# Optimization experiments

Hardware: AMD Instinct MI355X
Metric: run time of the kernel (lower is better)

The kernel has to match this reference:

```python
import jax, jax.numpy as jnp
import numpy as np
import math

NUM_HEADS = 16
HIDDEN = 1024
HEAD = HIDDEN // NUM_HEADS


def setup_inputs() -> dict:
    key = jax.random.key(0)
    ks = jax.random.split(key, 11)
    B, S, H = 2, 2048, HIDDEN
    s = 1.0 / math.sqrt(H)
    return {
        "q": jax.random.normal(ks[0], (B, S, H), jnp.float32),
        "k": jax.random.normal(ks[1], (B, S, H), jnp.float32),
        "v": jax.random.normal(ks[2], (B, S, H), jnp.float32),
        "Wq": jax.random.normal(ks[3], (H, H), jnp.float32) * s,
        "bq": jnp.zeros((H,), jnp.float32),
        "Wk": jax.random.normal(ks[4], (H, H), jnp.float32) * s,
        "bk": jnp.zeros((H,), jnp.float32),
        "Wv": jax.random.normal(ks[5], (H, H), jnp.float32) * s,
        "bv": jnp.zeros((H,), jnp.float32),
        "Wo": jax.random.normal(ks[6], (H, H), jnp.float32) * s,
        "bo": jnp.zeros((H,), jnp.float32),
    }


def reference(q, k, v, Wq, bq, Wk, bk, Wv, bv, Wo, bo):
    B, S, H = q.shape
    nh, hd = NUM_HEADS, HEAD
    # projections (torch Linear: x @ W.T + b)
    qp = (q @ Wq.T + bq).reshape(B, S, nh, hd).transpose(0, 2, 1, 3)  # [B,nh,S,hd]
    kp = (k @ Wk.T + bk).reshape(B, S, nh, hd).transpose(0, 2, 1, 3)
    vp = (v @ Wv.T + bv).reshape(B, S, nh, hd).transpose(0, 2, 1, 3)
    scores = jnp.einsum('bhqd,bhkd->bhqk', qp, kp) / math.sqrt(hd)
    attn = jax.nn.softmax(scores, axis=-1)  # [B,nh,S,S]
    o = jnp.einsum('bhqk,bhkd->bhqd', attn, vp)
    o = o.transpose(0, 2, 1, 3).reshape(B, S, H)
    return o @ Wo.T + bo
```

## Files before the change

### kernel.cpp

```cpp
#include <hip/hip_runtime.h>
#include <cstdint>
#include <type_traits>
#include <utility>

typedef __attribute__((ext_vector_type(8))) short short8;
typedef __attribute__((ext_vector_type(8))) _Float16 f16x8_t;
typedef __attribute__((ext_vector_type(4))) float f32x4;

template <typename V, typename = void>
struct mfma_h_takes : std::false_type {};
template <typename V>
struct mfma_h_takes<V, std::void_t<decltype(__builtin_amdgcn_mfma_f32_16x16x32_f16(
    std::declval<V>(), std::declval<V>(), std::declval<f32x4>(), 0, 0, 0))>>
    : std::true_type {};

using hfrag_t = std::conditional_t<mfma_h_takes<f16x8_t>::value, f16x8_t, short8>;
static_assert(mfma_h_takes<f16x8_t>::value || mfma_h_takes<short8>::value,
              "no usable mfma_f32_16x16x32_f16 signature");

__device__ __forceinline__ f32x4 mfma16h(hfrag_t a, hfrag_t b, f32x4 c) {
  return __builtin_amdgcn_mfma_f32_16x16x32_f16(a, b, c, 0, 0, 0);
}

__device__ __forceinline__ void gld_lds16(const void* g, void* l) {
  __builtin_amdgcn_global_load_lds(
      (const __attribute__((address_space(1))) void*)(uintptr_t)g,
      (__attribute__((address_space(3))) void*)(uint32_t)(uintptr_t)l, 16, 0, 0);
}

__device__ __forceinline__ uint16_t f16_rne(float x) {
  return __builtin_bit_cast(uint16_t, (_Float16)x);
}
__device__ __forceinline__ float f16_up(uint16_t h) {
  return (float)__builtin_bit_cast(_Float16, h);
}

__device__ __forceinline__ float exp2_fast(float x) {
#if __has_builtin(__builtin_amdgcn_exp2f)
  return __builtin_amdgcn_exp2f(x);
#else
  return exp2f(x);
#endif
}
__device__ __forceinline__ uint32_t pk_f16(float a, float b) {
#if __has_builtin(__builtin_amdgcn_cvt_pkrtz)
  return __builtin_bit_cast(uint32_t, __builtin_amdgcn_cvt_pkrtz(a, b));
#else
  union { uint16_t u[2]; uint32_t w; } r;
  r.u[0] = f16_rne(fminf(a, 65504.0f));
  r.u[1] = f16_rne(fminf(b, 65504.0f));
  return r.w;
#endif
}

__device__ __forceinline__ void lds_barrier() {
  asm volatile("s_waitcnt lgkmcnt(0)" ::: "memory");
  __builtin_amdgcn_sched_barrier(0);
  __builtin_amdgcn_s_barrier();
  __builtin_amdgcn_sched_barrier(0);
}

__device__ __forceinline__ int swz(int row, int col) {
  return row * 64 + ((((col >> 3) + row) & 7) << 3) + (col & 7);
}

struct SplitArgs {
  const float* src[4];
  uint16_t* hi[4];
  uint16_t* lo[4];
  int n4;
};
__global__ void split_multi(SplitArgs a) {
  const int z = blockIdx.y;
  int i = blockIdx.x * 256 + threadIdx.x;
  if (i >= a.n4) return;
  float4 x = ((const float4*)a.src[z])[i];
  ushort4 h;
  h.x = f16_rne(x.x);
  h.y = f16_rne(x.y);
  h.z = f16_rne(x.z);
  h.w = f16_rne(x.w);
  ((ushort4*)a.hi[z])[i] = h;
  if (a.lo[z]) {
    ushort4 l;
    l.x = f16_rne(x.x - f16_up(h.x));
    l.y = f16_rne(x.y - f16_up(h.y));
    l.z = f16_rne(x.z - f16_up(h.z));
    l.w = f16_rne(x.w - f16_up(h.w));
    ((ushort4*)a.lo[z])[i] = l;
  }
}

struct QKVArgs {
  const uint16_t* Ah[3];
  const uint16_t* Bh[3];
  const float* bias[3];
  uint16_t* oH[3];
  uint16_t* oL[3];
};

__global__ __launch_bounds__(256, 3) void gemm_qkv(QKVArgs args) {
  __shared__ uint16_t lds[2][2][128][32];
  const int K = 1024;
  const int tid = threadIdx.x;
  const int wv = tid >> 6, lane = tid & 63;
  const int lm = lane & 15, g = lane >> 4;
  const int wm = (wv & 1) * 64, wn = (wv >> 1) * 64;
  const int z = blockIdx.z;
  const bool isT = (z == 2);
  const int t = blockIdx.x + 8 * blockIdx.y;
  const int kx = t & 7, j = t >> 3;
  const int sx = (j & 3) | ((kx & 1) << 2);
  const int sy = (j >> 2) | ((kx >> 1) << 3);
  const int gm0 = (isT ? sx : sy) * 128;
  const int gn0 = (isT ? sy : sx) * 128;

  const uint16_t* base[2] = {args.Ah[z] + (size_t)gm0 * K,
                             args.Bh[z] + (size_t)gn0 * K};
  const int rl = lane >> 2;
  const int scl = (((lane & 3) - (rl >> 1)) & 3) * 8;
  const int ucol = ((g + (lm >> 1)) & 3) * 8;

  f32x4 acc[4][4];
#pragma unroll
  for (int a = 0; a < 4; ++a)
#pragma unroll
    for (int b = 0; b < 4; ++b) acc[a][b] = (f32x4)0.0f;

#pragma unroll
  for (int jj = 0; jj < 4; ++jj) {
    const int c = wv + 4 * jj;
    const int p = c >> 3, r16 = (c & 7) * 16;
    gld_lds16(base[p] + (size_t)(r16 + rl) * K + 0 + scl, &lds[0][p][r16][0]);
  }

#pragma unroll 1
  for (int ti = 0; ti < 32; ++ti) {
    const int cur = ti & 1;
    if (ti + 1 < 32) {
      const int kt = (ti + 1) * 32;
#pragma unroll
      for (int jj = 0; jj < 4; ++jj) {
        const int c = wv + 4 * jj;
        const int p = c >> 3, r16 = (c & 7) * 16;
        gld_lds16(base[p] + (size_t)(r16 + rl) * K + kt + scl,
                  &lds[cur ^ 1][p][r16][0]);
      }
      asm volatile("s_waitcnt vmcnt(4)" ::: "memory");
    } else {
      asm volatile("s_waitcnt vmcnt(0)" ::: "memory");
    }
    __builtin_amdgcn_sched_barrier(0);
    __builtin_amdgcn_s_barrier();
    __builtin_amdgcn_sched_barrier(0);
    hfrag_t af[4];
#pragma unroll
    for (int mf = 0; mf < 4; ++mf) {
      af[mf] = *(const hfrag_t*)&lds[cur][0][wm + mf * 16 + lm][ucol];
    }
#pragma unroll
    for (int nf = 0; nf < 4; ++nf) {
      hfrag_t bhf = *(const hfrag_t*)&lds[cur][1][wn + nf * 16 + lm][ucol];
#pragma unroll
      for (int mf = 0; mf < 4; ++mf) {
        acc[mf][nf] = mfma16h(af[mf], bhf, acc[mf][nf]);
      }
    }
    __builtin_amdgcn_sched_barrier(0);
    __builtin_amdgcn_s_barrier();
    __builtin_amdgcn_sched_barrier(0);
  }
  const float* bias = args.bias[z];
  uint16_t* oH = args.oH[z];
  uint16_t* oL = args.oL[z];
  const float kQScale = 0.18033688f;
#pragma unroll
  for (int mf = 0; mf < 4; ++mf) {
#pragma unroll
    for (int nf = 0; nf < 4; ++nf) {
      const int col = gn0 + wn + nf * 16 + lm;
#pragma unroll
      for (int i = 0; i < 4; ++i) {
        const int row = gm0 + wm + mf * 16 + g * 4 + i;
        float v = acc[mf][nf][i] + (isT ? bias[row] : bias[col]);
        if (z == 0) v *= kQScale;
        uint16_t h = f16_rne(v);
        size_t addr;
        if (!isT) {
          addr = ((size_t)((row >> 11) * 16 + (col >> 6)) * 2048 + (row & 2047)) * 64 +
                 (col & 63);
        } else {
          addr = ((size_t)((col >> 11) * 1024 + row)) * 2048 + (col & 2047);
        }
        oH[addr] = h;
        if (oL) oL[addr] = f16_rne(v - f16_up(h));
      }
    }
  }
}

__global__ __launch_bounds__(256, 2) void gemm_o(
    const uint16_t* __restrict__ Ah, const uint16_t* __restrict__ Bh,
    const float* __restrict__ bias, float* __restrict__ out) {
  const int K = 1024, N = 1024;
  __shared__ uint16_t ldsA[2][64][64];
  __shared__ uint16_t ldsB[2][128][64];
  const int tid = threadIdx.x;
  const int wv = tid >> 6, lane = tid & 63;
  const int lm = lane & 15, g = lane >> 4;
  const int wm = (wv & 1) * 32, wn = (wv >> 1) * 64;
  const int t = blockIdx.x + 8 * blockIdx.y;
  const int kx = t & 7, j = t >> 3;
  const int sx = (j & 3) | ((kx & 1) << 2);
  const int sy = (j >> 2) | ((kx >> 1) << 4);
  const int gm0 = sy * 64, gn0 = sx * 128;
  const uint16_t* baseA = Ah + (size_t)gm0 * K;
  const uint16_t* baseB = Bh + (size_t)gn0 * K;
  const int rl8 = lane >> 3;
  const int scl = (((lane & 7) - rl8) & 7) * 8;

  f32x4 acc[2][4];
#pragma unroll
  for (int a = 0; a < 2; ++a)
#pragma unroll
    for (int b = 0; b < 4; ++b) acc[a][b] = (f32x4)0.0f;

#pragma unroll
  for (int jj = 0; jj < 6; ++jj) {
    const int c = wv + 4 * jj;
    if (c < 8) {
      gld_lds16(baseA + (size_t)(c * 8 + rl8) * K + 0 + scl, &ldsA[0][c * 8][0]);
    } else {
      const int b = c - 8;
      gld_lds16(baseB + (size_t)(b * 8 + rl8) * K + 0 + scl, &ldsB[0][b * 8][0]);
    }
  }

#pragma unroll 1
  for (int ti = 0; ti < 16; ++ti) {
    const int cur = ti & 1;
    if (ti + 1 < 16) {
      const int kt = (ti + 1) * 64;
#pragma unroll
      for (int jj = 0; jj < 6; ++jj) {
        const int c = wv + 4 * jj;
        if (c < 8) {
          gld_lds16(baseA + (size_t)(c * 8 + rl8) * K + kt + scl,
                    &ldsA[cur ^ 1][c * 8][0]);
        } else {
          const int b = c - 8;
          gld_lds16(baseB + (size_t)(b * 8 + rl8) * K + kt + scl,
                    &ldsB[cur ^ 1][b * 8][0]);
        }
      }
      asm volatile("s_waitcnt vmcnt(6)" ::: "memory");
    } else {
      asm volatile("s_waitcnt vmcnt(0)" ::: "memory");
    }
    __builtin_amdgcn_sched_barrier(0);
    __builtin_amdgcn_s_barrier();
    __builtin_amdgcn_sched_barrier(0);
#pragma unroll
    for (int ks = 0; ks < 2; ++ks) {
      const int uc = ((ks * 4 + g + lm) & 7) * 8;
      hfrag_t af[2];
#pragma unroll
      for (int mf = 0; mf < 2; ++mf) {
        af[mf] = *(const hfrag_t*)&ldsA[cur][wm + mf * 16 + lm][uc];
      }
#pragma unroll
      for (int nf = 0; nf < 4; ++nf) {
        hfrag_t bhf = *(const hfrag_t*)&ldsB[cur][wn + nf * 16 + lm][uc];
#pragma unroll
        for (int mf = 0; mf < 2; ++mf) {
          acc[mf][nf] = mfma16h(af[mf], bhf, acc[mf][nf]);
        }
      }
    }
    __builtin_amdgcn_sched_barrier(0);
    __builtin_amdgcn_s_barrier();
    __builtin_amdgcn_sched_barrier(0);
  }
#pragma unroll
  for (int mf = 0; mf < 2; ++mf)
#pragma unroll
    for (int nf = 0; nf < 4; ++nf) {
      const int col = gn0 + wn + nf * 16 + lm;
#pragma unroll
      for (int i = 0; i < 4; ++i) {
        const int row = gm0 + wm + mf * 16 + g * 4 + i;
        out[(size_t)row * N + col] = acc[mf][nf][i] + bias[col];
      }
    }
}

__global__ __launch_bounds__(256, 2) void attn_kernel(
    const uint16_t* __restrict__ Qh,
    const uint16_t* __restrict__ Kh,
    const uint16_t* __restrict__ Vh,
    float* __restrict__ opart, float* __restrict__ lpart) {
  __shared__ uint16_t kt[4096];
  __shared__ uint16_t vt[4096];
  __shared__ uint16_t pp[8192];
  const int tid = threadIdx.x;
  const int wave = tid >> 6, lane = tid & 63;
  const int lm = lane & 15, g = lane >> 4;
  const int linear = blockIdx.x + 32 * blockIdx.y;
  const int bh = (linear & 7) + 8 * (linear >> 8);
  const int qt = (linear >> 3) & 15;
  const int half = (linear >> 7) & 1;
  const int kvh = half * 1024;
  const size_t base = (size_t)bh * 131072;
  const int q0 = qt * 128 + wave * 32;

  hfrag_t qf[2][2];
#pragma unroll
  for (int b = 0; b < 2; ++b) {
    const size_t rb = base + (size_t)(q0 + b * 16 + lm) * 64 + g * 8;
    qf[b][0] = *(const hfrag_t*)(Qh + rb);
    qf[b][1] = *(const hfrag_t*)(Qh + rb + 32);
  }
  f32x4 oacc[2][4];
  f32x4 lacc[2];
#pragma unroll
  for (int mf = 0; mf < 2; ++mf) {
    lacc[mf] = (f32x4)0.0f;
#pragma unroll
    for (int nf = 0; nf < 4; ++nf) oacc[mf][nf] = (f32x4)0.0f;
  }
  short8 ones_s = (short8)(short)0x3C00;
  hfrag_t ones = __builtin_bit_cast(hfrag_t, ones_s);

  const int sr = tid >> 3;
  const int sc = (tid & 7) * 8;

  uint4 kr0, kr1, vr0, vr1;
  {
    const size_t ka = base + (size_t)(kvh + sr) * 64 + sc;
    kr0 = *(const uint4*)(Kh + ka);
    kr1 = *(const uint4*)(Kh + ka + 2048);
  }

#pragma unroll 1
  for (int it = 0; it < 16; ++it) {
    const int kv0 = kvh + it * 64;
    *(uint4*)&kt[swz(sr, sc)] = kr0;
    *(uint4*)&kt[swz(sr + 32, sc)] = kr1;
    lds_barrier();
    {
      const size_t va = base + (size_t)sr * 2048 + kv0 + sc;
      vr0 = *(const uint4*)(Vh + va);
      vr1 = *(const uint4*)(Vh + va + 65536);
    }
    if (it + 1 < 16) {
      const size_t ka = base + (size_t)(kv0 + 64 + sr) * 64 + sc;
      kr0 = *(const uint4*)(Kh + ka);
      kr1 = *(const uint4*)(Kh + ka + 2048);
    }
    f32x4 sct[4][2];
#pragma unroll
    for (int a = 0; a < 4; ++a)
#pragma unroll
      for (int b = 0; b < 2; ++b) sct[a][b] = (f32x4)0.0f;
    __builtin_amdgcn_s_setprio(1);
#pragma unroll
    for (int ks = 0; ks < 2; ++ks) {
#pragma unroll
      for (int a = 0; a < 4; ++a) {
        hfrag_t kfh = *(const hfrag_t*)&kt[swz(a * 16 + lm, ks * 32 + g * 8)];
#pragma unroll
        for (int b = 0; b < 2; ++b) {
          sct[a][b] = mfma16h(kfh, qf[b][ks], sct[a][b]);
        }
      }
    }
    __builtin_amdgcn_s_setprio(0);
#pragma unroll
    for (int a = 0; a < 4; ++a) {
#pragma unroll
      for (int b = 0; b < 2; ++b) {
        float e0 = exp2_fast(sct[a][b][0]);
        float e1 = exp2_fast(sct[a][b][1]);
        float e2 = exp2_fast(sct[a][b][2]);
        float e3 = exp2_fast(sct[a][b][3]);
        uint2 pk;
        pk.x = pk_f16(e0, e1);
        pk.y = pk_f16(e2, e3);
        *(uint2*)&pp[swz(wave * 32 + b * 16 + lm, a * 16 + g * 4)] = pk;
      }
    }
    *(uint4*)&vt[swz(sr, sc)] = vr0;
    *(uint4*)&vt[swz(sr + 32, sc)] = vr1;
    lds_barrier();
    __builtin_amdgcn_s_setprio(1);
#pragma unroll
    for (int ks = 0; ks < 2; ++ks) {
      hfrag_t pa[2];
#pragma unroll
      for (int mf = 0; mf < 2; ++mf) {
        pa[mf] = *(const hfrag_t*)&pp[swz(wave * 32 + mf * 16 + lm, ks * 32 + g * 8)];
        lacc[mf] = mfma16h(pa[mf], ones, lacc[mf]);
      }
#pragma unroll
      for (int nf = 0; nf < 4; ++nf) {
        hfrag_t vbh = *(const hfrag_t*)&vt[swz(nf * 16 + lm, ks * 32 + g * 8)];
#pragma unroll
        for (int mf = 0; mf < 2; ++mf) {
          oacc[mf][nf] = mfma16h(pa[mf], vbh, oacc[mf][nf]);
        }
      }
    }
    __builtin_amdgcn_s_setprio(0);
  }
  const int obase = (half * 32 + bh) * 2048;
#pragma unroll
  for (int mf = 0; mf < 2; ++mf) {
#pragma unroll
    for (int i = 0; i < 4; ++i) {
      const int qrow = qt * 128 + wave * 32 + mf * 16 + g * 4 + i;
      float* orow = opart + ((size_t)obase + qrow) * 64;
#pragma unroll
      for (int nf = 0; nf < 4; ++nf) orow[nf * 16 + lm] = oacc[mf][nf][i];
      if (lm == 0) lpart[obase + qrow] = lacc[mf][i];
    }
  }
}

__global__ void combine_kernel(const float* __restrict__ opart,
                               const float* __restrict__ lpart,
                               uint16_t* __restrict__ oh) {
  const int idx = blockIdx.x * 256 + threadIdx.x;
  const float4 a = ((const float4*)opart)[idx];
  const float4 b = ((const float4*)(opart + 4194304))[idx];
  const int row = idx >> 4;
  const float linv = 1.0f / (lpart[row] + lpart[65536 + row]);
  const int bh = row >> 11, qq = row & 2047;
  const int bb = bh >> 4, hh = bh & 15;
  const size_t o = ((size_t)(bb * 2048 + qq)) * 1024 + hh * 64 + (idx & 15) * 4;
  ushort4 H;
  H.x = f16_rne((a.x + b.x) * linv);
  H.y = f16_rne((a.y + b.y) * linv);
  H.z = f16_rne((a.z + b.z) * linv);
  H.w = f16_rne((a.w + b.w) * linv);
  *(ushort4*)(oh + o) = H;
}

extern "C" void kernel_launch(void* const* d_in, const int* in_sizes, int n_in,
                              void* d_out, int out_size, void* d_ws, size_t ws_size,
                              hipStream_t stream) {
  const float* q = (const float*)d_in[0];
  const float* k = (const float*)d_in[1];
  const float* v = (const float*)d_in[2];
  const float* Wq = (const float*)d_in[3];
  const float* bq = (const float*)d_in[4];
  const float* Wk = (const float*)d_in[5];
  const float* bk = (const float*)d_in[6];
  const float* Wv = (const float*)d_in[7];
  const float* bv = (const float*)d_in[8];
  const float* Wo = (const float*)d_in[9];
  const float* bo = (const float*)d_in[10];

  const size_t NX = 4194304;
  const size_t NW = 1048576;
  uint16_t* p = (uint16_t*)d_ws;
  uint16_t* xqh = p; p += NX; uint16_t* xql = p; p += NX;
  uint16_t* xkh = p; p += NX; uint16_t* xkl = p; p += NX;
  uint16_t* xvh = p; p += NX; uint16_t* xvl = p; p += NX;
  uint16_t* wqh = p; p += NW; uint16_t* wql = p; p += NW;
  uint16_t* wkh = p; p += NW; uint16_t* wkl = p; p += NW;
  uint16_t* wvh = p; p += NW; uint16_t* wvl = p; p += NW;
  uint16_t* woh = p; p += NW; uint16_t* wol = p; p += NW;
  uint16_t* qph = p; p += NX; uint16_t* qpl = p; p += NX;
  uint16_t* kph = p; p += NX; uint16_t* kpl = p; p += NX;
  uint16_t* vth = p; p += NX; uint16_t* vtl = p; p += NX;
  uint16_t* oh = xqh;
  float* opart = (float*)xkh;
  float* lpart = opart + 2 * 4194304;

  SplitArgs sx;
  sx.src[0] = q;  sx.hi[0] = xqh; sx.lo[0] = nullptr;
  sx.src[1] = k;  sx.hi[1] = xkh; sx.lo[1] = nullptr;
  sx.src[2] = v;  sx.hi[2] = xvh; sx.lo[2] = nullptr;
  sx.src[3] = nullptr; sx.hi[3] = nullptr; sx.lo[3] = nullptr;
  sx.n4 = (int)(NX / 4);
  split_multi<<<dim3((unsigned)(NX / 4 / 256), 3), 256, 0, stream>>>(sx);

  SplitArgs sw;
  sw.src[0] = Wq; sw.hi[0] = wqh; sw.lo[0] = nullptr;
  sw.src[1] = Wk; sw.hi[1] = wkh; sw.lo[1] = nullptr;
  sw.src[2] = Wv; sw.hi[2] = wvh; sw.lo[2] = nullptr;
  sw.src[3] = Wo; sw.hi[3] = woh; sw.lo[3] = nullptr;
  sw.n4 = (int)(NW / 4);
  split_multi<<<dim3((unsigned)(NW / 4 / 256), 4), 256, 0, stream>>>(sw);

  QKVArgs qa;
  qa.Ah[0] = xqh; qa.Bh[0] = wqh; qa.bias[0] = bq; qa.oH[0] = qph; qa.oL[0] = nullptr;
  qa.Ah[1] = xkh; qa.Bh[1] = wkh; qa.bias[1] = bk; qa.oH[1] = kph; qa.oL[1] = nullptr;
  qa.Ah[2] = wvh; qa.Bh[2] = xvh; qa.bias[2] = bv; qa.oH[2] = vth; qa.oL[2] = nullptr;
  gemm_qkv<<<dim3(8, 32, 3), 256, 0, stream>>>(qa);

  attn_kernel<<<dim3(32, 32), 256, 0, stream>>>(qph, kph, vth, opart, lpart);
  combine_kernel<<<4096, 256, 0, stream>>>(opart, lpart, oh);

  gemm_o<<<dim3(8, 64), 256, 0, stream>>>(oh, woh, bo, (float*)d_out);
}
```

Measured before the change: 230.1 us.

## Halve attention query tile per block, merge split launches, drop lo-part plumbing

The attention kernel now gives each wave 16 query rows instead of 32, so each block covers 64 queries and the grid doubles to 2048 blocks. This shrinks registers and LDS per block, which should allow more resident blocks and finer load balance. The cost is that each K/V tile is loaded into LDS twice as often per query, and each K fragment feeds half as many MFMAs. The two fp32-to-fp16 split launches are merged into one 7-slice launch, where the weight slices exit early past their shorter length, and the unused low-part residual code is removed.

```diff
diff --git a/kernel.cpp b/kernel.cpp
--- a/kernel.cpp
+++ b/kernel.cpp
@@ -65,15 +65,14 @@
 }
 
 struct SplitArgs {
-  const float* src[4];
-  uint16_t* hi[4];
-  uint16_t* lo[4];
-  int n4;
+  const float* src[7];
+  uint16_t* hi[7];
+  int n4[7];
 };
 __global__ void split_multi(SplitArgs a) {
   const int z = blockIdx.y;
   int i = blockIdx.x * 256 + threadIdx.x;
-  if (i >= a.n4) return;
+  if (i >= a.n4[z]) return;
   float4 x = ((const float4*)a.src[z])[i];
   ushort4 h;
   h.x = f16_rne(x.x);
@@ -81,14 +80,6 @@
   h.z = f16_rne(x.z);
   h.w = f16_rne(x.w);
   ((ushort4*)a.hi[z])[i] = h;
-  if (a.lo[z]) {
-    ushort4 l;
-    l.x = f16_rne(x.x - f16_up(h.x));
-    l.y = f16_rne(x.y - f16_up(h.y));
-    l.z = f16_rne(x.z - f16_up(h.z));
-    l.w = f16_rne(x.w - f16_up(h.w));
-    ((ushort4*)a.lo[z])[i] = l;
-  }
 }
 
 struct QKVArgs {
@@ -96,7 +87,6 @@
   const uint16_t* Bh[3];
   const float* bias[3];
   uint16_t* oH[3];
-  uint16_t* oL[3];
 };
 
 __global__ __launch_bounds__(256, 3) void gemm_qkv(QKVArgs args) {
@@ -172,7 +162,6 @@
   }
   const float* bias = args.bias[z];
   uint16_t* oH = args.oH[z];
-  uint16_t* oL = args.oL[z];
   const float kQScale = 0.18033688f;
 #pragma unroll
   for (int mf = 0; mf < 4; ++mf) {
@@ -184,7 +173,6 @@
         const int row = gm0 + wm + mf * 16 + g * 4 + i;
         float v = acc[mf][nf][i] + (isT ? bias[row] : bias[col]);
         if (z == 0) v *= kQScale;
-        uint16_t h = f16_rne(v);
         size_t addr;
         if (!isT) {
           addr = ((size_t)((row >> 11) * 16 + (col >> 6)) * 2048 + (row & 2047)) * 64 +
@@ -192,8 +180,7 @@
         } else {
           addr = ((size_t)((col >> 11) * 1024 + row)) * 2048 + (col & 2047);
         }
-        oH[addr] = h;
-        if (oL) oL[addr] = f16_rne(v - f16_up(h));
+        oH[addr] = f16_rne(v);
       }
     }
   }
@@ -301,33 +288,28 @@
     float* __restrict__ opart, float* __restrict__ lpart) {
   __shared__ uint16_t kt[4096];
   __shared__ uint16_t vt[4096];
-  __shared__ uint16_t pp[8192];
+  __shared__ uint16_t pp[4096];
   const int tid = threadIdx.x;
   const int wave = tid >> 6, lane = tid & 63;
   const int lm = lane & 15, g = lane >> 4;
   const int linear = blockIdx.x + 32 * blockIdx.y;
-  const int bh = (linear & 7) + 8 * (linear >> 8);
-  const int qt = (linear >> 3) & 15;
-  const int half = (linear >> 7) & 1;
+  const int bh = (linear & 7) + 8 * (linear >> 9);
+  const int qt = (linear >> 3) & 31;
+  const int half = (linear >> 8) & 1;
   const int kvh = half * 1024;
   const size_t base = (size_t)bh * 131072;
-  const int q0 = qt * 128 + wave * 32;
-
-  hfrag_t qf[2][2];
-#pragma unroll
-  for (int b = 0; b < 2; ++b) {
-    const size_t rb = base + (size_t)(q0 + b * 16 + lm) * 64 + g * 8;
-    qf[b][0] = *(const hfrag_t*)(Qh + rb);
-    qf[b][1] = *(const hfrag_t*)(Qh + rb + 32);
-  }
-  f32x4 oacc[2][4];
-  f32x4 lacc[2];
-#pragma unroll
-  for (int mf = 0; mf < 2; ++mf) {
-    lacc[mf] = (f32x4)0.0f;
-#pragma unroll
-    for (int nf = 0; nf < 4; ++nf) oacc[mf][nf] = (f32x4)0.0f;
-  }
+  const int q0 = qt * 64 + wave * 16;
+
+  hfrag_t qf[2];
+  {
+    const size_t rb = base + (size_t)(q0 + lm) * 64 + g * 8;
+    qf[0] = *(const hfrag_t*)(Qh + rb);
+    qf[1] = *(const hfrag_t*)(Qh + rb + 32);
+  }
+  f32x4 oacc[4];
+  f32x4 lacc = (f32x4)0.0f;
+#pragma unroll
+  for (int nf = 0; nf < 4; ++nf) oacc[nf] = (f32x4)0.0f;
   short8 ones_s = (short8)(short)0x3C00;
   hfrag_t ones = __builtin_bit_cast(hfrag_t, ones_s);
 
@@ -357,37 +339,29 @@
       kr0 = *(const uint4*)(Kh + ka);
       kr1 = *(const uint4*)(Kh + ka + 2048);
     }
-    f32x4 sct[4][2];
-#pragma unroll
-    for (int a = 0; a < 4; ++a)
-#pragma unroll
-      for (int b = 0; b < 2; ++b) sct[a][b] = (f32x4)0.0f;
+    f32x4 sct[4];
+#pragma unroll
+    for (int a = 0; a < 4; ++a) sct[a] = (f32x4)0.0f;
     __builtin_amdgcn_s_setprio(1);
 #pragma unroll
     for (int ks = 0; ks < 2; ++ks) {
 #pragma unroll
       for (int a = 0; a < 4; ++a) {
         hfrag_t kfh = *(const hfrag_t*)&kt[swz(a * 16 + lm, ks * 32 + g * 8)];
-#pragma unroll
-        for (int b = 0; b < 2; ++b) {
-          sct[a][b] = mfma16h(kfh, qf[b][ks], sct[a][b]);
-        }
+        sct[a] = mfma16h(kfh, qf[ks], sct[a]);
       }
     }
     __builtin_amdgcn_s_setprio(0);
 #pragma unroll
     for (int a = 0; a < 4; ++a) {
-#pragma unroll
-      for (int b = 0; b < 2; ++b) {
-        float e0 = exp2_fast(sct[a][b][0]);
-        float e1 = exp2_fast(sct[a][b][1]);
-        float e2 = exp2_fast(sct[a][b][2]);
-        float e3 = exp2_fast(sct[a][b][3]);
-        uint2 pk;
-        pk.x = pk_f16(e0, e1);
-        pk.y = pk_f16(e2, e3);
-        *(uint2*)&pp[swz(wave * 32 + b * 16 + lm, a * 16 + g * 4)] = pk;
-      }
+      float e0 = exp2_fast(sct[a][0]);
+      float e1 = exp2_fast(sct[a][1]);
+      float e2 = exp2_fast(sct[a][2]);
+      float e3 = exp2_fast(sct[a][3]);
+      uint2 pk;
+      pk.x = pk_f16(e0, e1);
+      pk.y = pk_f16(e2, e3);
+      *(uint2*)&pp[swz(wave * 16 + lm, a * 16 + g * 4)] = pk;
     }
     *(uint4*)&vt[swz(sr, sc)] = vr0;
     *(uint4*)&vt[swz(sr + 32, sc)] = vr1;
@@ -395,34 +369,24 @@
     __builtin_amdgcn_s_setprio(1);
 #pragma unroll
     for (int ks = 0; ks < 2; ++ks) {
-      hfrag_t pa[2];
-#pragma unroll
-      for (int mf = 0; mf < 2; ++mf) {
-        pa[mf] = *(const hfrag_t*)&pp[swz(wave * 32 + mf * 16 + lm, ks * 32 + g * 8)];
-        lacc[mf] = mfma16h(pa[mf], ones, lacc[mf]);
-      }
+      hfrag_t pa = *(const hfrag_t*)&pp[swz(wave * 16 + lm, ks * 32 + g * 8)];
+      lacc = mfma16h(pa, ones, lacc);
 #pragma unroll
       for (int nf = 0; nf < 4; ++nf) {
         hfrag_t vbh = *(const hfrag_t*)&vt[swz(nf * 16 + lm, ks * 32 + g * 8)];
-#pragma unroll
-        for (int mf = 0; mf < 2; ++mf) {
-          oacc[mf][nf] = mfma16h(pa[mf], vbh, oacc[mf][nf]);
-        }
+        oacc[nf] = mfma16h(pa, vbh, oacc[nf]);
       }
     }
     __builtin_amdgcn_s_setprio(0);
   }
   const int obase = (half * 32 + bh) * 2048;
 #pragma unroll
-  for (int mf = 0; mf < 2; ++mf) {
-#pragma unroll
-    for (int i = 0; i < 4; ++i) {
-      const int qrow = qt * 128 + wave * 32 + mf * 16 + g * 4 + i;
-      float* orow = opart + ((size_t)obase + qrow) * 64;
-#pragma unroll
-      for (int nf = 0; nf < 4; ++nf) orow[nf * 16 + lm] = oacc[mf][nf][i];
-      if (lm == 0) lpart[obase + qrow] = lacc[mf][i];
-    }
+  for (int i = 0; i < 4; ++i) {
+    const int qrow = q0 + g * 4 + i;
+    float* orow = opart + ((size_t)obase + qrow) * 64;
+#pragma unroll
+    for (int nf = 0; nf < 4; ++nf) orow[nf * 16 + lm] = oacc[nf][i];
+    if (lm == 0) lpart[obase + qrow] = lacc[i];
   }
 }
 
@@ -477,29 +441,23 @@
   float* opart = (float*)xkh;
   float* lpart = opart + 2 * 4194304;
 
-  SplitArgs sx;
-  sx.src[0] = q;  sx.hi[0] = xqh; sx.lo[0] = nullptr;
-  sx.src[1] = k;  sx.hi[1] = xkh; sx.lo[1] = nullptr;
-  sx.src[2] = v;  sx.hi[2] = xvh; sx.lo[2] = nullptr;
-  sx.src[3] = nullptr; sx.hi[3] = nullptr; sx.lo[3] = nullptr;
-  sx.n4 = (int)(NX / 4);
-  split_multi<<<dim3((unsigned)(NX / 4 / 256), 3), 256, 0, stream>>>(sx);
-
-  SplitArgs sw;
-  sw.src[0] = Wq; sw.hi[0] = wqh; sw.lo[0] = nullptr;
-  sw.src[1] = Wk; sw.hi[1] = wkh; sw.lo[1] = nullptr;
-  sw.src[2] = Wv; sw.hi[2] = wvh; sw.lo[2] = nullptr;
-  sw.src[3] = Wo; sw.hi[3] = woh; sw.lo[3] = nullptr;
-  sw.n4 = (int)(NW / 4);
-  split_multi<<<dim3((unsigned)(NW / 4 / 256), 4), 256, 0, stream>>>(sw);
+  SplitArgs sa;
+  sa.src[0] = q;  sa.hi[0] = xqh; sa.n4[0] = (int)(NX / 4);
+  sa.src[1] = k;  sa.hi[1] = xkh; sa.n4[1] = (int)(NX / 4);
+  sa.src[2] = v;  sa.hi[2] = xvh; sa.n4[2] = (int)(NX / 4);
+  sa.src[3] = Wq; sa.hi[3] = wqh; sa.n4[3] = (int)(NW / 4);
+  sa.src[4] = Wk; sa.hi[4] = wkh; sa.n4[4] = (int)(NW / 4);
+  sa.src[5] = Wv; sa.hi[5] = wvh; sa.n4[5] = (int)(NW / 4);
+  sa.src[6] = Wo; sa.hi[6] = woh; sa.n4[6] = (int)(NW / 4);
+  split_multi<<<dim3((unsigned)(NX / 4 / 256), 7), 256, 0, stream>>>(sa);
 
   QKVArgs qa;
-  qa.Ah[0] = xqh; qa.Bh[0] = wqh; qa.bias[0] = bq; qa.oH[0] = qph; qa.oL[0] = nullptr;
-  qa.Ah[1] = xkh; qa.Bh[1] = wkh; qa.bias[1] = bk; qa.oH[1] = kph; qa.oL[1] = nullptr;
-  qa.Ah[2] = wvh; qa.Bh[2] = xvh; qa.bias[2] = bv; qa.oH[2] = vth; qa.oL[2] = nullptr;
+  qa.Ah[0] = xqh; qa.Bh[0] = wqh; qa.bias[0] = bq; qa.oH[0] = qph;
+  qa.Ah[1] = xkh; qa.Bh[1] = wkh; qa.bias[1] = bk; qa.oH[1] = kph;
+  qa.Ah[2] = wvh; qa.Bh[2] = xvh; qa.bias[2] = bv; qa.oH[2] = vth;
   gemm_qkv<<<dim3(8, 32, 3), 256, 0, stream>>>(qa);
 
-  attn_kernel<<<dim3(32, 32), 256, 0, stream>>>(qph, kph, vth, opart, lpart);
+  attn_kernel<<<dim3(32, 64), 256, 0, stream>>>(qph, kph, vth, opart, lpart);
   combine_kernel<<<4096, 256, 0, stream>>>(opart, lpart, oh);
 
   gemm_o<<<dim3(8, 64), 256, 0, stream>>>(oh, woh, bo, (float*)d_out);
```

Measured after the change: 237.4 us. 3.2% more time.
